# Kernel optimization log

Measured on AMD Instinct MI355X. Metric: run time of the kernel, lower is better.

Reference implementation:

```python
import jax, jax.numpy as jnp
import numpy as np

G = 4096   # num_genes
P = 4096   # num_perts
H = 64     # hidden_size
B = 4      # num_graphs
E1 = 81920 # coexpress edges
E2 = 81920 # GO edges
FF = 512   # transformer ffn
NH = 2     # attention heads
INTER, LAT = 32, 16  # VAE dims

def _bn(x, g, b, eps=1e-5):
    # BatchNorm1d in training mode: batch stats (biased var)
    m = x.mean(0); v = x.var(0)
    return (x - m) / jnp.sqrt(v + eps) * g + b

def _ln(x, g, b, eps=1e-5):
    m = x.mean(-1, keepdims=True); v = x.var(-1, keepdims=True)
    return (x - m) / jnp.sqrt(v + eps) * g + b

def _mlp2(x, w1, b1, g1, be1, w2, b2, g2, be2):
    # MLP([a,b,c]) builds Linear->BN->ReLU->Linear->BN (trailing ReLU stripped)
    h = jax.nn.relu(_bn(x @ w1.T + b1, g1, be1))
    return _bn(h @ w2.T + b2, g2, be2)

def _sgconv(x, ei, ew, w, b, n):
    # SGConv K=1: gcn_norm (self loops, symmetric norm) then linear
    src = jnp.concatenate([ei[0], jnp.arange(n)])
    dst = jnp.concatenate([ei[1], jnp.arange(n)])
    wgt = jnp.concatenate([ew, jnp.ones((n,), ew.dtype)])
    deg = jax.ops.segment_sum(wgt, dst, num_segments=n)
    dinv = jnp.where(deg > 0, 1.0 / jnp.sqrt(jnp.where(deg > 0, deg, 1.0)), 0.0)
    norm = dinv[dst] * wgt * dinv[src]
    agg = jax.ops.segment_sum(norm[:, None] * x[src], dst, num_segments=n)
    return agg @ w.T + b

def setup_inputs():
    ks = iter(jax.random.split(jax.random.key(0), 80))
    def nrm(shape, s=0.05):
        return jax.random.normal(next(ks), shape, dtype=jnp.float32) * s
    d = {}
    d['x'] = jax.random.uniform(next(ks), (B * G,), dtype=jnp.float32)
    d['pert_idx'] = jax.random.randint(next(ks), (B, 2), 0, P)
    d['mask'] = jnp.zeros((G, G), jnp.float32)
    d['ei_co'] = jax.random.randint(next(ks), (2, E1), 0, G)
    d['w_co'] = jax.random.uniform(next(ks), (E1,), dtype=jnp.float32)
    d['ei_go'] = jax.random.randint(next(ks), (2, E2), 0, P)
    d['w_go'] = jax.random.uniform(next(ks), (E2,), dtype=jnp.float32)
    d['gene_emb'] = nrm((G, H)); d['emb_pos'] = nrm((G, H)); d['pert_tbl'] = nrm((P, H))
    d['sg_co_w'] = nrm((H, H)); d['sg_co_b'] = jnp.zeros((H,))
    d['sg_go_w'] = nrm((H, H)); d['sg_go_b'] = jnp.zeros((H,))
    d['bn_emb_g'] = jnp.ones((H,)); d['bn_emb_b'] = jnp.zeros((H,))
    for pre, din, dout in [('etv2_1', H, H), ('etv2_2', H, H), ('pf_1', H, H), ('pf_2', H, H), ('rw_1', H, 2 * H), ('rw_2', 2 * H, H)]:
        d[pre + '_w'] = nrm((dout, din)); d[pre + '_b'] = jnp.zeros((dout,))
        d[pre + '_g'] = jnp.ones((dout,)); d[pre + '_be'] = jnp.zeros((dout,))
    d['bnpb_g'] = jnp.ones((H,)); d['bnpb_b'] = jnp.zeros((H,))
    d['attn_in_w'] = nrm((3 * H, H)); d['attn_in_b'] = jnp.zeros((3 * H,))
    d['attn_out_w'] = nrm((H, H)); d['attn_out_b'] = jnp.zeros((H,))
    d['ln1_g'] = jnp.ones((H,)); d['ln1_b'] = jnp.zeros((H,))
    d['ff1_w'] = nrm((FF, H)); d['ff1_b'] = jnp.zeros((FF,))
    d['ff2_w'] = nrm((H, FF)); d['ff2_b'] = jnp.zeros((H,))
    d['ln2_g'] = jnp.ones((H,)); d['ln2_b'] = jnp.zeros((H,))
    d['indv_w1'] = nrm((G, H)); d['indv_b1'] = jnp.zeros((G,))
    d['vae_e1_w'] = nrm((INTER, G)); d['vae_e1_b'] = jnp.zeros((INTER,))
    d['vae_mu_w'] = nrm((LAT, INTER)); d['vae_mu_b'] = jnp.zeros((LAT,))
    d['vae_lv_w'] = nrm((LAT, INTER)); d['vae_lv_b'] = jnp.zeros((LAT,))
    d['vae_d1_w'] = nrm((INTER, LAT)); d['vae_d1_b'] = jnp.zeros((INTER,))
    d['vae_d2_w'] = nrm((G, INTER)); d['vae_d2_b'] = jnp.zeros((G,))
    d['eps'] = jax.random.normal(next(ks), (B, LAT), dtype=jnp.float32)
    return d

def reference(x, pert_idx, mask, ei_co, w_co, ei_go, w_go, gene_emb, emb_pos, pert_tbl, sg_co_w, sg_co_b, sg_go_w, sg_go_b, bn_emb_g, bn_emb_b, etv2_1_w, etv2_1_b, etv2_1_g, etv2_1_be, etv2_2_w, etv2_2_b, etv2_2_g, etv2_2_be, pf_1_w, pf_1_b, pf_1_g, pf_1_be, pf_2_w, pf_2_b, pf_2_g, pf_2_be, rw_1_w, rw_1_b, rw_1_g, rw_1_be, rw_2_w, rw_2_b, rw_2_g, rw_2_be, bnpb_g, bnpb_b, attn_in_w, attn_in_b, attn_out_w, attn_out_b, ln1_g, ln1_b, ff1_w, ff1_b, ff2_w, ff2_b, ln2_g, ln2_b, indv_w1, indv_b1, vae_e1_w, vae_e1_b, vae_mu_w, vae_mu_b, vae_lv_w, vae_lv_b, vae_d1_w, vae_d1_b, vae_d2_w, vae_d2_b, eps):
    # gene base embedding (identical across graphs until pert fusion)
    base = jax.nn.relu(_bn(gene_emb, bn_emb_g, bn_emb_b))               # [G,H]
    pos = _sgconv(emb_pos, ei_co, w_co, sg_co_w, sg_co_b, G)            # 1 gene-GNN layer
    base = base + 0.2 * pos
    base = _mlp2(base, etv2_1_w, etv2_1_b, etv2_1_g, etv2_1_be, etv2_2_w, etv2_2_b, etv2_2_g, etv2_2_be)
    # pert embeddings propagated on GO graph
    pge = _sgconv(pert_tbl, ei_go, w_go, sg_go_w, sg_go_b, P)           # [P,H]
    # per-graph pert_track: sum of pert embeddings (all pert_idx valid)
    psum = pge[pert_idx].sum(axis=1)                                    # [B,H]
    etot = _mlp2(psum, pf_1_w, pf_1_b, pf_1_g, pf_1_be, pf_2_w, pf_2_b, pf_2_g, pf_2_be)
    base_b = base[None, :, :] + etot[:, None, :]                        # [B,G,H]
    flat = jax.nn.relu(_bn(base_b.reshape(B * G, H), bnpb_g, bnpb_b))
    out = _mlp2(flat, rw_1_w, rw_1_b, rw_1_g, rw_1_be, rw_2_w, rw_2_b, rw_2_g, rw_2_be)
    out = out.reshape(B, G, H)
    # transformer encoder layer (post-norm, relu, nhead=2), eval/no-dropout
    qkv = out @ attn_in_w.T + attn_in_b
    q, k, v = jnp.split(qkv, 3, axis=-1)
    hd = H // NH
    q = q.reshape(B, G, NH, hd); k = k.reshape(B, G, NH, hd); v = v.reshape(B, G, NH, hd)
    sc = jnp.einsum('bqhd,bkhd->bhqk', q, k) / np.float32(np.sqrt(hd)) + mask
    a = jax.nn.softmax(sc, axis=-1)
    ctx = jnp.einsum('bhqk,bkhd->bqhd', a, v).reshape(B, G, H)
    att = ctx @ attn_out_w.T + attn_out_b
    h1 = _ln(out + att, ln1_g, ln1_b)
    ff = jax.nn.relu(h1 @ ff1_w.T + ff1_b) @ ff2_w.T + ff2_b
    enc = _ln(h1 + ff, ln2_g, ln2_b)
    # per-gene linear: (enc.unsqueeze(-1)*indv_w1).sum(2)+indv_b1
    pred0 = jnp.einsum('bgh,gh->bg', enc, indv_w1) + indv_b1
    # VAE branch on raw expression
    xr = x.reshape(B, G)
    he = jax.nn.relu(xr @ vae_e1_w.T + vae_e1_b)
    mu = he @ vae_mu_w.T + vae_mu_b
    lv = he @ vae_lv_w.T + vae_lv_b
    z = mu + eps * jnp.exp(0.5 * lv)
    hdc = jax.nn.relu(z @ vae_d1_w.T + vae_d1_b)
    recon = hdc @ vae_d2_w.T + vae_d2_b
    kl = -0.5 * jnp.mean(jnp.sum(1.0 + lv - mu ** 2 - jnp.exp(lv), axis=1))
    recon = jnp.where(xr == 0, 0.0, recon)
    pred = pred0 + recon
    return (pred, kl)
```

## Files before the change

kernel.cpp:

```cpp
#include <hip/hip_runtime.h>
#include <hip/hip_bf16.h>
#include <math.h>

#define GG 4096
#define PP 4096
#define HH 64
#define BB 4
#define E1N 81920
#define E2N 81920
#define FFD 512
#define BNEPS 1e-5f
#define LOG2E 1.44269504088896341f
#define QPRE (0.17677669529663687f * LOG2E)

typedef unsigned short ushort_t;
typedef unsigned int uint_t;
using sh8 = __attribute__((ext_vector_type(8))) short;
using sh4 = __attribute__((ext_vector_type(4))) short;
using f4  = __attribute__((ext_vector_type(4))) float;

#if __has_builtin(__builtin_amdgcn_mfma_f32_16x16x16bf16_1k)
#define MFMA16(a, b, c) __builtin_amdgcn_mfma_f32_16x16x16bf16_1k((a), (b), (c), 0, 0, 0)
#elif __has_builtin(__builtin_amdgcn_mfma_f32_16x16x16_bf16)
#define MFMA16(a, b, c) __builtin_amdgcn_mfma_f32_16x16x16_bf16((a), (b), (c), 0, 0, 0)
#else
static __device__ inline f4 mfma16_asm(sh4 a, sh4 b, f4 c) {
    f4 d;
    asm volatile("v_mfma_f32_16x16x16_bf16 %0, %1, %2, %3"
                 : "=v"(d) : "v"(a), "v"(b), "v"(c));
    return d;
}
#define MFMA16(a, b, c) mfma16_asm((a), (b), (c))
#endif

#define OF_STATS   0
#define OF_DEGCO   2048
#define OF_DEGGO   6144
#define OF_PSLOT   10240
#define OF_ETOT    10752
#define OF_HDC     11008
#define OF_HE      11136
#define OF_MFLAG   11264
#define OF_CNT     12288
#define OF_OFFS    16384
#define OF_WOFF    20608
#define OF_SSRC    24704
#define OF_SNRM    106624
#define OF_BASEIN  274432
#define OF_Y1      536576
#define OF_Y2      798720
#define OF_FLAT    1060864
#define OF_RW1     2109440
#define OF_RW2     4206592
#define OF_OUT     5255168
#define OF_QKV     6303744
#define OF_QB      12288
#define OF_KB      (OF_QB + 524288)
#define OF_VF      OF_FLAT
#define OF_OPA     OF_QKV
#define OF_OPB     OF_OUT
#define OF_LP      OF_RW1
#define OPS        1048576
#define OF_W1B     9449472
#define OF_W2B     9465856

__device__ inline ushort_t f2b(float f) {
    uint_t u = __builtin_bit_cast(uint_t, f);
    u += 0x7FFFu + ((u >> 16) & 1u);
    return (ushort_t)(u >> 16);
}

__device__ inline void gld16(const void* gptr, void* lptr) {
    __builtin_amdgcn_global_load_lds(
        (const __attribute__((address_space(1))) uint_t*)gptr,
        (__attribute__((address_space(3))) uint_t*)lptr, 16, 0, 0);
}

__device__ void dev_vae_he(int bid, const float* __restrict__ x, const float* __restrict__ W,
                           const float* __restrict__ bias, float* he, float* sh) {
    int b = bid >> 5, i = bid & 31;
    float s = 0.f;
    for (int g = threadIdx.x; g < 4096; g += 256) s += x[b * 4096 + g] * W[i * 4096 + g];
    sh[threadIdx.x] = s;
    __syncthreads();
    for (int o = 128; o > 0; o >>= 1) {
        if (threadIdx.x < o) sh[threadIdx.x] += sh[threadIdx.x + o];
        __syncthreads();
    }
    if (threadIdx.x == 0) he[b * 32 + i] = fmaxf(sh[0] + bias[i], 0.f);
}

__device__ void dev_vae_mid(const float* __restrict__ he,
                            const float* __restrict__ muw, const float* __restrict__ mub,
                            const float* __restrict__ lvw, const float* __restrict__ lvb,
                            const float* __restrict__ d1w, const float* __restrict__ d1b,
                            const float* __restrict__ eps, float* hdc, float* klout, float* zs) {
    int t = threadIdx.x;
    if (t < 64) {
        int b = t >> 4, l = t & 15;
        float mu = mub[l], lv = lvb[l];
        for (int i = 0; i < 32; i++) {
            float hv = he[b * 32 + i];
            mu += hv * muw[l * 32 + i];
            lv += hv * lvw[l * 32 + i];
        }
        zs[t] = mu + eps[t] * expf(0.5f * lv);
        float kterm = 1.f + lv - mu * mu - expf(lv);
        for (int o = 32; o > 0; o >>= 1) kterm += __shfl_xor(kterm, o, 64);
        if (t == 0) klout[0] = -0.5f * kterm * 0.25f;
    }
    __syncthreads();
    if (t < 128) {
        int b = t >> 5, i = t & 31;
        float a = d1b[i];
        for (int l = 0; l < 16; l++) a += zs[b * 16 + l] * d1w[i * 16 + l];
        hdc[t] = fmaxf(a, 0.f);
    }
}

__device__ void dev_edge_deg(int bid, const int* __restrict__ ei, const float* __restrict__ w,
                             float* deg, int E, int* cnt) {
    int e = bid * 256 + threadIdx.x;
    if (e < E) {
        int d = ei[E + e];
        atomicAdd(&deg[d], w[e]);
        if (cnt) atomicAdd(&cnt[d], 1);
    }
}

__device__ void dev_cs_part(int bid, const float* __restrict__ X, int N,
                            float* sum, float* sumsq, float* sh) {
    int t = threadIdx.x;
    int col = t & 63, ro = t >> 6;
    int rows = N >> 8;
    int r0 = bid * rows;
    float s = 0.f, q = 0.f;
    for (int r = r0 + ro; r < r0 + rows; r += 4) {
        float v = X[r * 64 + col];
        s += v; q += v * v;
    }
    float* ls = sh; float* lq = sh + 256;
    ls[t] = s; lq[t] = q;
    __syncthreads();
    if (t < 64) {
        for (int j = t + 64; j < 256; j += 64) { s += ls[j]; q += lq[j]; }
        atomicAdd(&sum[t], s);
        atomicAdd(&sumsq[t], q);
    }
}

__device__ void dev_mask_scan(int bid, const float* __restrict__ mask, int* flag) {
    const uint4* m4 = (const uint4*)mask;
    const int total = (GG * GG) / 4;
    uint_t acc = 0u;
    for (int i = bid * 256 + threadIdx.x; i < total; i += 512 * 256) {
        uint4 v = m4[i];
        acc |= v.x | v.y | v.z | v.w;
    }
    if (acc) atomicOr(flag, 1);
}

__device__ void dev_scatter(int bid, const int* __restrict__ ei, const float* __restrict__ w,
                            const float* __restrict__ deg,
                            int* woff, int* ssrc, float* snrm) {
    int e = bid * 256 + threadIdx.x;
    if (e >= E1N) return;
    int src = ei[e], dst = ei[E1N + e];
    float nrm = rsqrtf(deg[dst] + 1.f) * w[e] * rsqrtf(deg[src] + 1.f);
    int pos = atomicAdd(&woff[dst], 1);
    ssrc[pos] = src;
    snrm[pos] = nrm;
}
// ... 340 lines not shown
        float eb = etot[bb * 64 + t];
        bsc[t] = sc2 * is3 * g3[t];
        bsh[t] = (sh2 + eb - m3) * is3 * g3[t] + b3[t];
    }
    __syncthreads();
    for (int i = t; i < 1024; i += 256) {
        int r = i >> 4, kq = (i & 15) * 4;
        int g = (row0 + r) & 4095;
        float4 v = *(const float4*)&y2[(size_t)g * 64 + kq];
        Xs[r][kq] = fmaxf(v.x * bsc[kq] + bsh[kq], 0.f);
        Xs[r][kq + 1] = fmaxf(v.y * bsc[kq + 1] + bsh[kq + 1], 0.f);
        Xs[r][kq + 2] = fmaxf(v.z * bsc[kq + 2] + bsh[kq + 2], 0.f);
        Xs[r][kq + 3] = fmaxf(v.w * bsc[kq + 3] + bsh[kq + 3], 0.f);
        float4 wv = *(const float4*)&W[(size_t)(cb + r) * 64 + kq];
        Ws[r][kq] = wv.x; Ws[r][kq + 1] = wv.y; Ws[r][kq + 2] = wv.z; Ws[r][kq + 3] = wv.w;
    }
    __syncthreads();
    float acc[4][4];
    #pragma unroll
    for (int j = 0; j < 4; j++)
        #pragma unroll
        for (int i = 0; i < 4; i++) acc[j][i] = 0.f;
    #pragma unroll 4
    for (int k = 0; k < 64; k += 2) {
        float2 a[4], b[4];
        #pragma unroll
        for (int j = 0; j < 4; j++) a[j] = *(const float2*)&Xs[r0 + j][k];
        #pragma unroll
        for (int i = 0; i < 4; i++) b[i] = *(const float2*)&Ws[c0 + i][k];
        #pragma unroll
        for (int j = 0; j < 4; j++)
            #pragma unroll
            for (int i = 0; i < 4; i++)
                acc[j][i] += a[j].x * b[i].x + a[j].y * b[i].y;
    }
    float4 bi = *(const float4*)&bias[cb + c0];
    float scol[4] = {0.f, 0.f, 0.f, 0.f}, qcol[4] = {0.f, 0.f, 0.f, 0.f};
    #pragma unroll
    for (int j = 0; j < 4; j++) {
        float4 o;
        o.x = acc[j][0] + bi.x; o.y = acc[j][1] + bi.y;
        o.z = acc[j][2] + bi.z; o.w = acc[j][3] + bi.w;
        *(float4*)&Y[(size_t)(row0 + r0 + j) * 128 + cb + c0] = o;
        scol[0] += o.x; scol[1] += o.y; scol[2] += o.z; scol[3] += o.w;
        qcol[0] += o.x * o.x; qcol[1] += o.y * o.y;
        qcol[2] += o.z * o.z; qcol[3] += o.w * o.w;
    }
    __syncthreads();
    #pragma unroll
    for (int i = 0; i < 4; i++) { Xs[ty][c0 + i] = scol[i]; Ws[ty][c0 + i] = qcol[i]; }
    __syncthreads();
    if (t < 64) {
        float ss = 0.f, qq = 0.f;
        #pragma unroll
        for (int r = 0; r < 16; r++) { ss += Xs[r][t]; qq += Ws[r][t]; }
        atomicAdd(&osum[cb + t], ss);
        atomicAdd(&osq[cb + t], qq);
    }
}

__launch_bounds__(256)
__global__ void k_gemm_qkv(const float* __restrict__ X, const float* __restrict__ W,
                           const float* __restrict__ bias,
                           const float* __restrict__ bnsum, const float* __restrict__ bnsq,
                           const float* __restrict__ bng, const float* __restrict__ bnb,
                           ushort_t* __restrict__ Qb, ushort_t* __restrict__ Kb,
                           ushort_t* __restrict__ Vf) {
    __shared__ float Xs[64][66];
    __shared__ float Ws[64][66];
    __shared__ float bsc[64], bsh[64];
    const int t = threadIdx.x;
    const int row0 = blockIdx.x * 64, yb = blockIdx.y, cb = yb * 64;
    const int tx = t & 15, ty = t >> 4;
    const int c0 = tx * 4, r0 = ty * 4;
    const float invN = 1.0f / (float)(BB * GG);
    if (t < 64) {
        float m = bnsum[t] * invN;
        float is_ = rsqrtf(bnsq[t] * invN - m * m + BNEPS);
        float sc = is_ * bng[t];
        bsc[t] = sc; bsh[t] = bnb[t] - m * sc;
    }
    __syncthreads();
    for (int i = t; i < 1024; i += 256) {
        int r = i >> 4, kq = (i & 15) * 4;
        float4 v = *(const float4*)&X[(size_t)(row0 + r) * 64 + kq];
        Xs[r][kq] = v.x * bsc[kq] + bsh[kq];
        Xs[r][kq + 1] = v.y * bsc[kq + 1] + bsh[kq + 1];
        Xs[r][kq + 2] = v.z * bsc[kq + 2] + bsh[kq + 2];
        Xs[r][kq + 3] = v.w * bsc[kq + 3] + bsh[kq + 3];
        float4 wv = *(const float4*)&W[(size_t)(cb + r) * 64 + kq];
        Ws[r][kq] = wv.x; Ws[r][kq + 1] = wv.y; Ws[r][kq + 2] = wv.z; Ws[r][kq + 3] = wv.w;
    }
    __syncthreads();
    float acc[4][4];
    #pragma unroll
    for (int j = 0; j < 4; j++)
        #pragma unroll
        for (int i = 0; i < 4; i++) acc[j][i] = 0.f;
    #pragma unroll 4
    for (int k = 0; k < 64; k += 2) {
        float2 a[4], b[4];
        #pragma unroll
        for (int j = 0; j < 4; j++) a[j] = *(const float2*)&Xs[r0 + j][k];
        #pragma unroll
        for (int i = 0; i < 4; i++) b[i] = *(const float2*)&Ws[c0 + i][k];
        #pragma unroll
        for (int j = 0; j < 4; j++)
            #pragma unroll
            for (int i = 0; i < 4; i++)
                acc[j][i] += a[j].x * b[i].x + a[j].y * b[i].y;
    }
    float4 bi = *(const float4*)&bias[cb + c0];
    const int b2 = row0 >> 12, tile = (row0 & 4095) >> 6;
    if (yb < 2) {
        ushort_t* Dst = (yb == 0) ? Qb : Kb;
        const float sc2 = (yb == 0) ? QPRE : 1.0f;
        const int h = c0 >> 5, d = c0 & 31;
        #pragma unroll
        for (int j = 0; j < 4; j++) {
            union { ushort_t u[4]; uint2 v; } pk;
            pk.u[0] = f2b((acc[j][0] + bi.x) * sc2);
            pk.u[1] = f2b((acc[j][1] + bi.y) * sc2);
            pk.u[2] = f2b((acc[j][2] + bi.z) * sc2);
            pk.u[3] = f2b((acc[j][3] + bi.w) * sc2);
            int g = (row0 & 4095) + r0 + j;
            *(uint2*)&Dst[((size_t)(b2 * 2 + h) * GG + g) * 32 + d] = pk.v;
        }
    } else {
        __syncthreads();
        #pragma unroll
        for (int j = 0; j < 4; j++) {
            Xs[r0 + j][c0] = acc[j][0] + bi.x;
            Xs[r0 + j][c0 + 1] = acc[j][1] + bi.y;
            Xs[r0 + j][c0 + 2] = acc[j][2] + bi.z;
            Xs[r0 + j][c0 + 3] = acc[j][3] + bi.w;
        }
        __syncthreads();
        #pragma unroll
        for (int h = 0; h < 2; h++) {
            union { ushort_t u[8]; uint4 v; } pk;
            #pragma unroll
            for (int j = 0; j < 8; j++) {
                int idx = t * 8 + j;
                int g2 = idx >> 8, L = (idx >> 2) & 63, i = idx & 3;
                int key = (g2 >> 1) * 16 + ((L >> 4) << 2) + i;
                int d = ((g2 & 1) << 4) + (L & 15);
                pk.u[j] = f2b(Xs[key][h * 32 + d]);
            }
            *(uint4*)&Vf[((size_t)((b2 * 2 + h) * 64 + tile)) * 2048 + t * 8] = pk.v;
        }
    }
}

__launch_bounds__(512, 4)
__global__ void k_attn_mfma(const ushort_t* __restrict__ Qb, const ushort_t* __restrict__ Kb,
                            const ushort_t* __restrict__ Vf, const float* __restrict__ mask,
                            const float* __restrict__ mflag,
                            float* __restrict__ opA, float* __restrict__ opB,
                            float* __restrict__ Lp) {
    __shared__ ushort_t Kl[2][4][2048];
    __shared__ ushort_t Vl[2][4][2048];
    const int split = blockIdx.y;
    const int bh0 = blockIdx.z * 4;
    const int q0 = blockIdx.x * 64;
    const int kstart = split * (GG / 4), kend = kstart + (GG / 4);
    const int t = threadIdx.x;
    const int lane = t & 63, w = t >> 6;
    const int qg = w >> 1, kh = w & 1;
    const int l15 = lane & 15, quad = lane >> 4;
    const int i2a = kh * 2, i2b = kh * 2 + 1;
    const int um = (*(const int*)mflag) != 0;

    sh8 qf[4];
    #pragma unroll
    for (int bh = 0; bh < 4; bh++)
        qf[bh] = *(const sh8*)&Qb[((size_t)(bh0 + bh) * GG + q0 + qg * 16 + l15) * 32 + quad * 8];
    const float* mrow = mask + (size_t)(q0 + qg * 16 + l15) * GG + quad * 4;

    auto stage = [&](int buf, int k0) {
        #pragma unroll
        for (int s = 0; s < 2; s++) {
            int idx = s * 512 + t;
            int bh = idx >> 8, c = idx & 255;
            int key = ((c >> 6) << 4) + (c & 15);
            int chunk = (c >> 4) & 3;
            gld16(Kb + ((size_t)(bh0 + bh) * GG + k0 + key) * 32 + chunk * 8,
                  &Kl[buf][bh][c * 8]);
            gld16(Vf + ((size_t)((bh0 + bh) * 64 + (k0 >> 6))) * 2048 + c * 8,
                  &Vl[buf][bh][c * 8]);
        }
    };
    stage(0, kstart);

    const float4 zf4 = {0.f, 0.f, 0.f, 0.f};
    float4 mva = zf4, mvb = zf4;
    if (um) {
        mva = *(const float4*)&mrow[kstart + i2a * 16];
        mvb = *(const float4*)&mrow[kstart + i2b * 16];
    }

    f4 O0[4], O1[4];
    float ls[4];
    #pragma unroll
    for (int bh = 0; bh < 4; bh++) {
        O0[bh] = f4{0.f, 0.f, 0.f, 0.f};
        O1[bh] = f4{0.f, 0.f, 0.f, 0.f};
        ls[bh] = 0.f;
    }

    for (int k0 = kstart; k0 < kend; k0 += 64) {
        const int cur = ((k0 - kstart) >> 6) & 1;
        __syncthreads();
        if (k0 + 64 < kend) stage(cur ^ 1, k0 + 64);
        float4 mva_n = zf4, mvb_n = zf4;
        if (um) {
            const int kp = (k0 + 64 < kend) ? (k0 + 64) : k0;
            mva_n = *(const float4*)&mrow[kp + i2a * 16];
            mvb_n = *(const float4*)&mrow[kp + i2b * 16];
        }
        #pragma unroll
        for (int bh = 0; bh < 4; bh++) {
            sh8 kfa = *(const sh8*)&Kl[cur][bh][(i2a * 64 + lane) * 8];
            sh8 kfb = *(const sh8*)&Kl[cur][bh][(i2b * 64 + lane) * 8];
            f4 z = {0.f, 0.f, 0.f, 0.f};
            f4 sa = __builtin_amdgcn_mfma_f32_16x16x32_bf16(kfa, qf[bh], z, 0, 0, 0);
            f4 sb = __builtin_amdgcn_mfma_f32_16x16x32_bf16(kfb, qf[bh], z, 0, 0, 0);
            {
                float p0 = exp2f(fmaf(mva.x, LOG2E, sa[0]));
                float p1 = exp2f(fmaf(mva.y, LOG2E, sa[1]));
                float p2 = exp2f(fmaf(mva.z, LOG2E, sa[2]));
                float p3 = exp2f(fmaf(mva.w, LOG2E, sa[3]));
                ls[bh] += (p0 + p1) + (p2 + p3);
                union { __hip_bfloat162 h2[2]; sh4 v; } pkp;
                pkp.h2[0] = __float22bfloat162_rn(float2{p0, p1});
                pkp.h2[1] = __float22bfloat162_rn(float2{p2, p3});
                sh4 vf0 = *(const sh4*)&Vl[cur][bh][((i2a * 2 + 0) * 64 + lane) * 4];
                sh4 vf1 = *(const sh4*)&Vl[cur][bh][((i2a * 2 + 1) * 64 + lane) * 4];
                O0[bh] = MFMA16(pkp.v, vf0, O0[bh]);
                O1[bh] = MFMA16(pkp.v, vf1, O1[bh]);
            }
            {
                float p0 = exp2f(fmaf(mvb.x, LOG2E, sb[0]));
                float p1 = exp2f(fmaf(mvb.y, LOG2E, sb[1]));
                float p2 = exp2f(fmaf(mvb.z, LOG2E, sb[2]));
                float p3 = exp2f(fmaf(mvb.w, LOG2E, sb[3]));
                ls[bh] += (p0 + p1) + (p2 + p3);
                union { __hip_bfloat162 h2[2]; sh4 v; } pkp;
                pkp.h2[0] = __float22bfloat162_rn(float2{p0, p1});
                pkp.h2[1] = __float22bfloat162_rn(float2{p2, p3});
                sh4 vf0 = *(const sh4*)&Vl[cur][bh][((i2b * 2 + 0) * 64 + lane) * 4];
                sh4 vf1 = *(const sh4*)&Vl[cur][bh][((i2b * 2 + 1) * 64 + lane) * 4];
                O0[bh] = MFMA16(pkp.v, vf0, O0[bh]);
                O1[bh] = MFMA16(pkp.v, vf1, O1[bh]);
            }
        }
        mva = mva_n; mvb = mvb_n;
    }
    #pragma unroll
    for (int bh = 0; bh < 4; bh++) {
        ls[bh] += __shfl_xor(ls[bh], 16, 64);
        ls[bh] += __shfl_xor(ls[bh], 32, 64);
    }
    __syncthreads();
    float* Ox = (float*)&Kl[0][0][0];
    float* Lx = (float*)&Vl[0][0][0];
    if (kh == 0) {
        #pragma unroll
        for (int bh = 0; bh < 4; bh++) {
            #pragma unroll
            for (int r = 0; r < 4; r++) {
                int ql = qg * 16 + quad * 4 + r;
                Ox[(bh * 64 + ql) * 32 + l15] = O0[bh][r];
                Ox[(bh * 64 + ql) * 32 + l15 + 16] = O1[bh][r];
            }
            if (quad == 0) Lx[bh * 64 + qg * 16 + l15] = ls[bh];
        }
    }
    __syncthreads();
    if (kh == 1) {
        float* op = (split < 3) ? (opA + (size_t)split * OPS) : opB;
        #pragma unroll
        for (int bh = 0; bh < 4; bh++) {
            int gbh = bh0 + bh;
            #pragma unroll
            for (int r = 0; r < 4; r++) {
                int ql = qg * 16 + quad * 4 + r;
                size_t o = ((size_t)gbh * GG + q0 + ql) * 32 + l15;
                op[o] = O0[bh][r] + Ox[(bh * 64 + ql) * 32 + l15];
                op[o + 16] = O1[bh][r] + Ox[(bh * 64 + ql) * 32 + l15 + 16];
            }
            if (quad == 0)
                Lp[split * 32768 + gbh * GG + q0 + qg * 16 + l15] =
                    ls[bh] + Lx[bh * 64 + qg * 16 + l15];
        }
    }
}

__launch_bounds__(256)
__global__ void k_tail(const float* __restrict__ opA, const float* __restrict__ opB,
                       const float* __restrict__ Lp, const float* __restrict__ yrw2,
                       const float* __restrict__ Waout, const float* __restrict__ baout,
                       const float* __restrict__ bsum5, const float* __restrict__ bsq5,
                       const float* __restrict__ bg5, const float* __restrict__ bb5,
                       const float* __restrict__ lg1, const float* __restrict__ lb1,
                       const ushort_t* __restrict__ W1b, const float* __restrict__ b1f,
                       const ushort_t* __restrict__ W2b, const float* __restrict__ b2f,
                       const float* __restrict__ lg2, const float* __restrict__ lb2,
                       const float* __restrict__ indvw, const float* __restrict__ indvb,
                       const float* __restrict__ hdc, const float* __restrict__ d2w,
                       const float* __restrict__ d2b, const float* __restrict__ x,
                       float* __restrict__ outp) {
    __shared__ float Wt[4160];
    __shared__ float Cs[4160];
    __shared__ ushort_t Hb[4096];
    __shared__ ushort_t FT[32768];
    __shared__ ushort_t WS[2][4096];
    const int t = threadIdx.x;
    const int r0b = blockIdx.x * 64;
    const int lane = t & 63, w = t >> 6;
    const int l15 = lane & 15, quad = lane >> 4;

    for (int i = t; i < 4096; i += 256) Wt[(i & 63) * 65 + (i >> 6)] = Waout[i];
    {
        int col = t & 63, rl = t >> 6;
        int hh = col >> 5, d = col & 31;
        for (int jj = 0; jj < 16; jj++) {
            int lrow = rl + jj * 4;
            int row = r0b + lrow;
            int b = row >> 12, q = row & 4095;
            int bhq = (b * 2 + hh) * GG + q;
            size_t oi = (size_t)bhq * 32 + d;
            float num = opA[oi] + opA[OPS + oi] + opA[2 * OPS + oi] + opB[oi];
            float den = Lp[bhq] + Lp[32768 + bhq] + Lp[65536 + bhq] + Lp[98304 + bhq];
            Cs[lrow * 65 + col] = num / den;
        }
    }
    __syncthreads();
    const float invN = 1.0f / (float)(BB * GG);
    float m5 = bsum5[lane] * invN;
    float is5 = rsqrtf(bsq5[lane] * invN - m5 * m5 + BNEPS);
    float h1v[16];
    for (int j = 0; j < 16; j++) {
        int lrow = w * 16 + j;
        int row = r0b + lrow;
        float acc = baout[lane];
        const float* cr = Cs + lrow * 65;
        #pragma unroll 8
        for (int k = 0; k < 64; k++) acc += cr[k] * Wt[k * 65 + lane];
        float ov = (yrw2[(size_t)row * 64 + lane] - m5) * is5 * bg5[lane] + bb5[lane];
        float v = ov + acc;
        float s = v;
        for (int o = 32; o > 0; o >>= 1) s += __shfl_xor(s, o, 64);
        float mean = s * (1.f / 64.f);
        float d = v - mean;
        float sq = d * d;
        for (int o = 32; o > 0; o >>= 1) sq += __shfl_xor(sq, o, 64);
        float inv = rsqrtf(sq * (1.f / 64.f) + BNEPS);
        h1v[j] = d * inv * lg1[lane] + lb1[lane];
    }
    __syncthreads();
    float* h1f = Wt;
    for (int j = 0; j < 16; j++) h1f[(w * 16 + j) * 65 + lane] = h1v[j];
    __syncthreads();
    if (t < 128) {
        int kt = t >> 6, lane6 = t & 63;
        int q2 = (lane6 >> 4) & 3, r15 = lane6 & 15;
        for (int rg = 0; rg < 4; rg++) {
            union { ushort_t u[8]; uint4 v4; } pk;
            #pragma unroll
            for (int j = 0; j < 8; j++)
                pk.u[j] = f2b(h1f[(rg * 16 + r15) * 65 + kt * 32 + q2 * 8 + j]);
            *(uint4*)&Hb[(rg * 2 + kt) * 512 + lane6 * 8] = pk.v4;
        }
    }
    auto stage1 = [&](int buf, int cb8) {
        int cb = cb8 * 64;
        #pragma unroll
        for (int kt = 0; kt < 2; kt++)
            gld16(W1b + (size_t)((cb + w * 16 + l15) * 64 + kt * 32 + quad * 8),
                  &WS[buf][(w * 2 + kt) * 512 + lane * 8]);
    };
    stage1(0, 0);
    for (int cb8 = 0; cb8 < 8; cb8++) {
        const int cur = cb8 & 1;
        __syncthreads();
        if (cb8 + 1 < 8) stage1(cur ^ 1, cb8 + 1);
        sh8 xf0 = *(const sh8*)&Hb[(w * 2 + 0) * 512 + lane * 8];
        sh8 xf1 = *(const sh8*)&Hb[(w * 2 + 1) * 512 + lane * 8];
        const int cb = cb8 * 64;
        #pragma unroll
        for (int c = 0; c < 4; c++) {
            sh8 wf0 = *(const sh8*)&WS[cur][(c * 2 + 0) * 512 + lane * 8];
            sh8 wf1 = *(const sh8*)&WS[cur][(c * 2 + 1) * 512 + lane * 8];
            f4 z = {0.f, 0.f, 0.f, 0.f};
            f4 acc = __builtin_amdgcn_mfma_f32_16x16x32_bf16(wf0, xf0, z, 0, 0, 0);
            acc = __builtin_amdgcn_mfma_f32_16x16x32_bf16(wf1, xf1, acc, 0, 0, 0);
            float4 bv = *(const float4*)&b1f[cb + c * 16 + quad * 4];
            union { ushort_t u[4]; uint2 v2; } pk;
            pk.u[0] = f2b(fmaxf(acc[0] + bv.x, 0.f));
            pk.u[1] = f2b(fmaxf(acc[1] + bv.y, 0.f));
            pk.u[2] = f2b(fmaxf(acc[2] + bv.z, 0.f));
            pk.u[3] = f2b(fmaxf(acc[3] + bv.w, 0.f));
            int kt512 = cb8 * 2 + (c >> 1);
            int quadp = (c & 1) * 2 + (quad >> 1);
            int j0 = (quad & 1) * 4;
            *(uint2*)&FT[((w * 16 + kt512) * 64 + quadp * 16 + l15) * 8 + j0] = pk.v2;
        }
    }
    auto stage2 = [&](int buf, int k0) {
        #pragma unroll
        for (int kt = 0; kt < 2; kt++)
            gld16(W2b + (size_t)((w * 16 + l15) * 512 + k0 + kt * 32 + quad * 8),
                  &WS[buf][(w * 2 + kt) * 512 + lane * 8]);
    };
    stage2(0, 0);
    f4 acc2[4];
    #pragma unroll
    for (int c = 0; c < 4; c++) acc2[c] = f4{0.f, 0.f, 0.f, 0.f};
    for (int k0 = 0; k0 < 512; k0 += 64) {
        const int cur = (k0 >> 6) & 1;
        __syncthreads();
        if (k0 + 64 < 512) stage2(cur ^ 1, k0 + 64);
        const int ktb = k0 >> 5;
        #pragma unroll
        for (int kt = 0; kt < 2; kt++) {
            sh8 xf = *(const sh8*)&FT[((w * 16 + ktb + kt) * 64 + lane) * 8];
            #pragma unroll
            for (int c = 0; c < 4; c++) {
                sh8 wf = *(const sh8*)&WS[cur][(c * 2 + kt) * 512 + lane * 8];
                acc2[c] = __builtin_amdgcn_mfma_f32_16x16x32_bf16(wf, xf, acc2[c], 0, 0, 0);
            }
        }
    }
    const int row = r0b + w * 16 + l15;
    const int b = row >> 12, g = row & 4095;
// ... 14 lines not shown
    sq += __shfl_xor(sq, 16, 64); sq += __shfl_xor(sq, 32, 64);
    float mean = s * (1.f / 64.f);
    float inv = rsqrtf(sq * (1.f / 64.f) - mean * mean + BNEPS);
    float pd = 0.f;
    #pragma unroll
    for (int c = 0; c < 4; c++) {
        float4 lgv = *(const float4*)&lg2[c * 16 + quad * 4];
        float4 lbv = *(const float4*)&lb2[c * 16 + quad * 4];
        float4 iwv = *(const float4*)&indvw[(size_t)g * 64 + c * 16 + quad * 4];
        pd += ((v[c][0] - mean) * inv * lgv.x + lbv.x) * iwv.x;
        pd += ((v[c][1] - mean) * inv * lgv.y + lbv.y) * iwv.y;
        pd += ((v[c][2] - mean) * inv * lgv.z + lbv.z) * iwv.z;
        pd += ((v[c][3] - mean) * inv * lgv.w + lbv.w) * iwv.w;
    }
    float rc = 0.f;
    #pragma unroll
    for (int i = 0; i < 8; i++)
        rc += hdc[b * 32 + quad * 8 + i] * d2w[(size_t)g * 32 + quad * 8 + i];
    pd += __shfl_xor(pd, 16, 64); pd += __shfl_xor(pd, 32, 64);
    rc += __shfl_xor(rc, 16, 64); rc += __shfl_xor(rc, 32, 64);
    if (quad == 0) {
        float recon = rc + d2b[g];
        if (x[row] == 0.f) recon = 0.f;
        outp[row] = pd + indvb[g] + recon;
    }
}

extern "C" void kernel_launch(void* const* d_in, const int* in_sizes, int n_in,
                              void* d_out, int out_size, void* d_ws, size_t ws_size,
                              hipStream_t stream) {
    const float* x        = (const float*)d_in[0];
    const int*   pert_idx = (const int*)  d_in[1];
    const float* mask     = (const float*)d_in[2];
    const int*   ei_co    = (const int*)  d_in[3];
    const float* w_co     = (const float*)d_in[4];
    const int*   ei_go    = (const int*)  d_in[5];
    const float* w_go     = (const float*)d_in[6];
    const float* gene_emb = (const float*)d_in[7];
    const float* emb_pos  = (const float*)d_in[8];
    const float* pert_tbl = (const float*)d_in[9];
    const float* sg_co_w  = (const float*)d_in[10];
    const float* sg_co_b  = (const float*)d_in[11];
    const float* sg_go_w  = (const float*)d_in[12];
    const float* sg_go_b  = (const float*)d_in[13];
    const float* bn_emb_g = (const float*)d_in[14];
    const float* bn_emb_b = (const float*)d_in[15];
    const float* etv1_w   = (const float*)d_in[16];
    const float* etv1_b   = (const float*)d_in[17];
    const float* etv1_g   = (const float*)d_in[18];
    const float* etv1_be  = (const float*)d_in[19];
    const float* etv2_w   = (const float*)d_in[20];
    const float* etv2_b   = (const float*)d_in[21];
    const float* etv2_g   = (const float*)d_in[22];
    const float* etv2_be  = (const float*)d_in[23];
    const float* pf1_w    = (const float*)d_in[24];
    const float* pf1_b    = (const float*)d_in[25];
    const float* pf1_g    = (const float*)d_in[26];
    const float* pf1_be   = (const float*)d_in[27];
    const float* pf2_w    = (const float*)d_in[28];
    const float* pf2_b    = (const float*)d_in[29];
    const float* pf2_g    = (const float*)d_in[30];
    const float* pf2_be   = (const float*)d_in[31];
    const float* rw1_w    = (const float*)d_in[32];
    const float* rw1_b    = (const float*)d_in[33];
    const float* rw1_g    = (const float*)d_in[34];
    const float* rw1_be   = (const float*)d_in[35];
    const float* rw2_w    = (const float*)d_in[36];
    const float* rw2_b    = (const float*)d_in[37];
    const float* rw2_g    = (const float*)d_in[38];
    const float* rw2_be   = (const float*)d_in[39];
    const float* bnpb_g   = (const float*)d_in[40];
    const float* bnpb_b   = (const float*)d_in[41];
    const float* ain_w    = (const float*)d_in[42];
    const float* ain_b    = (const float*)d_in[43];
    const float* aout_w   = (const float*)d_in[44];
    const float* aout_b   = (const float*)d_in[45];
    const float* ln1_g    = (const float*)d_in[46];
    const float* ln1_b    = (const float*)d_in[47];
    const float* ff1_w    = (const float*)d_in[48];
    const float* ff1_b    = (const float*)d_in[49];
    const float* ff2_w    = (const float*)d_in[50];
    const float* ff2_b    = (const float*)d_in[51];
    const float* ln2_g    = (const float*)d_in[52];
    const float* ln2_b    = (const float*)d_in[53];
    const float* indv_w   = (const float*)d_in[54];
    const float* indv_b   = (const float*)d_in[55];
    const float* ve1_w    = (const float*)d_in[56];
    const float* ve1_b    = (const float*)d_in[57];
    const float* vmu_w    = (const float*)d_in[58];
    const float* vmu_b    = (const float*)d_in[59];
    const float* vlv_w    = (const float*)d_in[60];
    const float* vlv_b    = (const float*)d_in[61];
    const float* vd1_w    = (const float*)d_in[62];
    const float* vd1_b    = (const float*)d_in[63];
    const float* vd2_w    = (const float*)d_in[64];
    const float* vd2_b    = (const float*)d_in[65];
    const float* veps     = (const float*)d_in[66];

    float* ws   = (float*)d_ws;
    float* outp = (float*)d_out;

    float* stm1 = ws + OF_STATS + 1 * 256; float* sti1 = stm1 + 128;
    float* stm2 = ws + OF_STATS + 2 * 256; float* sti2 = stm2 + 128;
    float* stm4 = ws + OF_STATS + 4 * 256; float* sti4 = stm4 + 128;
    float* stm5 = ws + OF_STATS + 5 * 256; float* sti5 = stm5 + 128;

    float* basein = ws + OF_BASEIN;
    float* y1     = ws + OF_Y1;
    float* y2     = ws + OF_Y2;
    float* yrw1   = ws + OF_RW1;
    float* yrw2   = ws + OF_RW2;
    float* opA    = ws + OF_OPA;
    float* opB    = ws + OF_OPB;
    float* Lp     = ws + OF_LP;
    ushort_t* Qb  = (ushort_t*)(ws + OF_QB);
    ushort_t* Kb  = (ushort_t*)(ws + OF_KB);
    ushort_t* Vf  = (ushort_t*)(ws + OF_VF);
    ushort_t* W1b = (ushort_t*)(ws + OF_W1B);
    ushort_t* W2b = (ushort_t*)(ws + OF_W2B);

    const int NG = BB * GG;
    const float iG = 1.0f / (float)GG, iNG = 1.0f / (float)NG;

    hipMemsetAsync(ws, 0, 11268 * sizeof(float), stream);
    hipMemsetAsync(ws + OF_CNT, 0, 4096 * sizeof(int), stream);

    k_fat12<<<1792, 256, 0, stream>>>(ws, ei_co, w_co, ei_go, w_go, gene_emb,
                                      x, ve1_w, ve1_b, ff1_w, ff2_w, mask);
    k_scan<<<1, 256, 0, stream>>>(ws);
    k_fat3<<<641, 256, 0, stream>>>(ws, ei_co, w_co, pert_idx,
                                    ei_go, w_go, pert_tbl,
                                    vmu_w, vmu_b, vlv_w, vlv_b, vd1_w, vd1_b,
                                    veps, outp + NG);
    k_fat4<<<1025, 256, 0, stream>>>(ws, gene_emb, emb_pos, sg_co_w, sg_co_b,
                                     bn_emb_g, bn_emb_b, pert_idx, pert_tbl,
                                     sg_go_w, sg_go_b,
                                     pf1_w, pf1_b, pf1_g, pf1_be,
                                     pf2_w, pf2_b, pf2_g, pf2_be);
    k_gemm64<<<dim3(GG / 64, 1), 256, 0, stream>>>(basein, etv1_w, etv1_b, y1, 64, 64,
                                                   nullptr, nullptr, nullptr, nullptr, 0.f, 0,
                                                   stm1, sti1);
    k_gemm64<<<dim3(GG / 64, 1), 256, 0, stream>>>(y1, etv2_w, etv2_b, y2, 64, 64,
                                                   stm1, sti1, etv1_g, etv1_be, iG, 1,
                                                   stm2, sti2);
    k_gemm_rw1<<<dim3(NG / 64, 2), 256, 0, stream>>>(y2, ws + OF_ETOT, stm2, sti2,
                                                     etv2_g, etv2_be, bnpb_g, bnpb_b,
                                                     rw1_w, rw1_b, yrw1, stm4, sti4);
    k_gemm64<<<dim3(NG / 64, 1), 256, 0, stream>>>(yrw1, rw2_w, rw2_b, yrw2, 128, 64,
                                                   stm4, sti4, rw1_g, rw1_be, iNG, 1,
                                                   stm5, sti5);
    k_gemm_qkv<<<dim3(NG / 64, 3), 256, 0, stream>>>(yrw2, ain_w, ain_b,
                                                     stm5, sti5, rw2_g, rw2_be,
                                                     Qb, Kb, Vf);
    k_attn_mfma<<<dim3(GG / 64, 4, 2), 512, 0, stream>>>(Qb, Kb, Vf, mask,
                                                         ws + OF_MFLAG, opA, opB, Lp);
    k_tail<<<NG / 64, 256, 0, stream>>>(opA, opB, Lp, yrw2, aout_w, aout_b,
                                        stm5, sti5, rw2_g, rw2_be, ln1_g, ln1_b,
                                        W1b, ff1_b, W2b, ff2_b, ln2_g, ln2_b,
                                        indv_w, indv_b, ws + OF_HDC, vd2_w, vd2_b,
                                        x, outp);
}
```

Baseline: 454.1 us.

## Halve heads per attention block and specialize mask-free softmax path

Each attention block now handles 2 batch-heads instead of 4. This halves the shared memory and register footprint, and the grid doubles along z to keep total work the same. Launch bounds rise to 8 blocks per CU so more blocks can be resident. The main loop is also templated on whether the mask is used, so the mask-free path skips the mask loads and the FMA before each exp2. In exchange, each K/V tile is loaded for fewer heads per block and the Q fragments are reused less.

```diff
diff --git a/kernel.cpp b/kernel.cpp
--- a/kernel.cpp
+++ b/kernel.cpp
@@ -18,6 +18,9 @@
 using sh8 = __attribute__((ext_vector_type(8))) short;
 using sh4 = __attribute__((ext_vector_type(4))) short;
 using f4  = __attribute__((ext_vector_type(4))) float;
+
+struct MaskOn  { static constexpr bool v = true; };
+struct MaskOff { static constexpr bool v = false; };
 
 #if __has_builtin(__builtin_amdgcn_mfma_f32_16x16x16bf16_1k)
 #define MFMA16(a, b, c) __builtin_amdgcn_mfma_f32_16x16x16bf16_1k((a), (b), (c), 0, 0, 0)
@@ -664,16 +667,16 @@
     }
 }
 
-__launch_bounds__(512, 4)
+__launch_bounds__(512, 8)
 __global__ void k_attn_mfma(const ushort_t* __restrict__ Qb, const ushort_t* __restrict__ Kb,
                             const ushort_t* __restrict__ Vf, const float* __restrict__ mask,
                             const float* __restrict__ mflag,
                             float* __restrict__ opA, float* __restrict__ opB,
                             float* __restrict__ Lp) {
-    __shared__ ushort_t Kl[2][4][2048];
-    __shared__ ushort_t Vl[2][4][2048];
+    __shared__ ushort_t Kl[2][2][2048];
+    __shared__ ushort_t Vl[2][2][2048];
     const int split = blockIdx.y;
-    const int bh0 = blockIdx.z * 4;
+    const int bh0 = blockIdx.z * 2;
     const int q0 = blockIdx.x * 64;
     const int kstart = split * (GG / 4), kend = kstart + (GG / 4);
     const int t = threadIdx.x;
@@ -683,93 +686,105 @@
     const int i2a = kh * 2, i2b = kh * 2 + 1;
     const int um = (*(const int*)mflag) != 0;
 
-    sh8 qf[4];
-    #pragma unroll
-    for (int bh = 0; bh < 4; bh++)
+    sh8 qf[2];
+    #pragma unroll
+    for (int bh = 0; bh < 2; bh++)
         qf[bh] = *(const sh8*)&Qb[((size_t)(bh0 + bh) * GG + q0 + qg * 16 + l15) * 32 + quad * 8];
     const float* mrow = mask + (size_t)(q0 + qg * 16 + l15) * GG + quad * 4;
 
     auto stage = [&](int buf, int k0) {
-        #pragma unroll
-        for (int s = 0; s < 2; s++) {
-            int idx = s * 512 + t;
-            int bh = idx >> 8, c = idx & 255;
-            int key = ((c >> 6) << 4) + (c & 15);
-            int chunk = (c >> 4) & 3;
-            gld16(Kb + ((size_t)(bh0 + bh) * GG + k0 + key) * 32 + chunk * 8,
-                  &Kl[buf][bh][c * 8]);
-            gld16(Vf + ((size_t)((bh0 + bh) * 64 + (k0 >> 6))) * 2048 + c * 8,
-                  &Vl[buf][bh][c * 8]);
-        }
+        int bh = t >> 8, c = t & 255;
+        int key = ((c >> 6) << 4) + (c & 15);
+        int chunk = (c >> 4) & 3;
+        gld16(Kb + ((size_t)(bh0 + bh) * GG + k0 + key) * 32 + chunk * 8,
+              &Kl[buf][bh][c * 8]);
+        gld16(Vf + ((size_t)((bh0 + bh) * 64 + (k0 >> 6))) * 2048 + c * 8,
+              &Vl[buf][bh][c * 8]);
     };
     stage(0, kstart);
 
-    const float4 zf4 = {0.f, 0.f, 0.f, 0.f};
-    float4 mva = zf4, mvb = zf4;
-    if (um) {
-        mva = *(const float4*)&mrow[kstart + i2a * 16];
-        mvb = *(const float4*)&mrow[kstart + i2b * 16];
-    }
-
-    f4 O0[4], O1[4];
-    float ls[4];
-    #pragma unroll
-    for (int bh = 0; bh < 4; bh++) {
+    f4 O0[2], O1[2];
+    float ls[2];
+    #pragma unroll
+    for (int bh = 0; bh < 2; bh++) {
         O0[bh] = f4{0.f, 0.f, 0.f, 0.f};
         O1[bh] = f4{0.f, 0.f, 0.f, 0.f};
         ls[bh] = 0.f;
     }
 
-    for (int k0 = kstart; k0 < kend; k0 += 64) {
-        const int cur = ((k0 - kstart) >> 6) & 1;
-        __syncthreads();
-        if (k0 + 64 < kend) stage(cur ^ 1, k0 + 64);
-        float4 mva_n = zf4, mvb_n = zf4;
-        if (um) {
-            const int kp = (k0 + 64 < kend) ? (k0 + 64) : k0;
-            mva_n = *(const float4*)&mrow[kp + i2a * 16];
-            mvb_n = *(const float4*)&mrow[kp + i2b * 16];
-        }
-        #pragma unroll
-        for (int bh = 0; bh < 4; bh++) {
-            sh8 kfa = *(const sh8*)&Kl[cur][bh][(i2a * 64 + lane) * 8];
-            sh8 kfb = *(const sh8*)&Kl[cur][bh][(i2b * 64 + lane) * 8];
-            f4 z = {0.f, 0.f, 0.f, 0.f};
-            f4 sa = __builtin_amdgcn_mfma_f32_16x16x32_bf16(kfa, qf[bh], z, 0, 0, 0);
-            f4 sb = __builtin_amdgcn_mfma_f32_16x16x32_bf16(kfb, qf[bh], z, 0, 0, 0);
-            {
-                float p0 = exp2f(fmaf(mva.x, LOG2E, sa[0]));
-                float p1 = exp2f(fmaf(mva.y, LOG2E, sa[1]));
-                float p2 = exp2f(fmaf(mva.z, LOG2E, sa[2]));
-                float p3 = exp2f(fmaf(mva.w, LOG2E, sa[3]));
-                ls[bh] += (p0 + p1) + (p2 + p3);
-                union { __hip_bfloat162 h2[2]; sh4 v; } pkp;
-                pkp.h2[0] = __float22bfloat162_rn(float2{p0, p1});
-                pkp.h2[1] = __float22bfloat162_rn(float2{p2, p3});
-                sh4 vf0 = *(const sh4*)&Vl[cur][bh][((i2a * 2 + 0) * 64 + lane) * 4];
-                sh4 vf1 = *(const sh4*)&Vl[cur][bh][((i2a * 2 + 1) * 64 + lane) * 4];
-                O0[bh] = MFMA16(pkp.v, vf0, O0[bh]);
-                O1[bh] = MFMA16(pkp.v, vf1, O1[bh]);
+    auto run = [&](auto tag) {
+        constexpr bool U = decltype(tag)::v;
+        const float4 zf4 = {0.f, 0.f, 0.f, 0.f};
+        float4 mva = zf4, mvb = zf4;
+        if constexpr (U) {
+            mva = *(const float4*)&mrow[kstart + i2a * 16];
+            mvb = *(const float4*)&mrow[kstart + i2b * 16];
+        }
+        for (int k0 = kstart; k0 < kend; k0 += 64) {
+            const int cur = ((k0 - kstart) >> 6) & 1;
+            __syncthreads();
+            if (k0 + 64 < kend) stage(cur ^ 1, k0 + 64);
+            float4 mva_n = zf4, mvb_n = zf4;
+            if constexpr (U) {
+                const int kp = (k0 + 64 < kend) ? (k0 + 64) : k0;
+                mva_n = *(const float4*)&mrow[kp + i2a * 16];
+                mvb_n = *(const float4*)&mrow[kp + i2b * 16];
             }
-            {
-                float p0 = exp2f(fmaf(mvb.x, LOG2E, sb[0]));
-                float p1 = exp2f(fmaf(mvb.y, LOG2E, sb[1]));
-                float p2 = exp2f(fmaf(mvb.z, LOG2E, sb[2]));
-                float p3 = exp2f(fmaf(mvb.w, LOG2E, sb[3]));
-                ls[bh] += (p0 + p1) + (p2 + p3);
-                union { __hip_bfloat162 h2[2]; sh4 v; } pkp;
-                pkp.h2[0] = __float22bfloat162_rn(float2{p0, p1});
-                pkp.h2[1] = __float22bfloat162_rn(float2{p2, p3});
-                sh4 vf0 = *(const sh4*)&Vl[cur][bh][((i2b * 2 + 0) * 64 + lane) * 4];
-                sh4 vf1 = *(const sh4*)&Vl[cur][bh][((i2b * 2 + 1) * 64 + lane) * 4];
-                O0[bh] = MFMA16(pkp.v, vf0, O0[bh]);
-                O1[bh] = MFMA16(pkp.v, vf1, O1[bh]);
+            #pragma unroll
+            for (int bh = 0; bh < 2; bh++) {
+                sh8 kfa = *(const sh8*)&Kl[cur][bh][(i2a * 64 + lane) * 8];
+                sh8 kfb = *(const sh8*)&Kl[cur][bh][(i2b * 64 + lane) * 8];
+                f4 z = {0.f, 0.f, 0.f, 0.f};
+                f4 sa = __builtin_amdgcn_mfma_f32_16x16x32_bf16(kfa, qf[bh], z, 0, 0, 0);
+                f4 sb = __builtin_amdgcn_mfma_f32_16x16x32_bf16(kfb, qf[bh], z, 0, 0, 0);
+                {
+                    float p0, p1, p2, p3;
+                    if constexpr (U) {
+                        p0 = exp2f(fmaf(mva.x, LOG2E, sa[0]));
+                        p1 = exp2f(fmaf(mva.y, LOG2E, sa[1]));
+                        p2 = exp2f(fmaf(mva.z, LOG2E, sa[2]));
+                        p3 = exp2f(fmaf(mva.w, LOG2E, sa[3]));
+                    } else {
+                        p0 = exp2f(sa[0]); p1 = exp2f(sa[1]);
+                        p2 = exp2f(sa[2]); p3 = exp2f(sa[3]);
+                    }
+                    ls[bh] += (p0 + p1) + (p2 + p3);
+                    union { __hip_bfloat162 h2[2]; sh4 v; } pkp;
+                    pkp.h2[0] = __float22bfloat162_rn(float2{p0, p1});
+                    pkp.h2[1] = __float22bfloat162_rn(float2{p2, p3});
+                    sh4 vf0 = *(const sh4*)&Vl[cur][bh][((i2a * 2 + 0) * 64 + lane) * 4];
+                    sh4 vf1 = *(const sh4*)&Vl[cur][bh][((i2a * 2 + 1) * 64 + lane) * 4];
+                    O0[bh] = MFMA16(pkp.v, vf0, O0[bh]);
+                    O1[bh] = MFMA16(pkp.v, vf1, O1[bh]);
+                }
+                {
+                    float p0, p1, p2, p3;
+                    if constexpr (U) {
+                        p0 = exp2f(fmaf(mvb.x, LOG2E, sb[0]));
+                        p1 = exp2f(fmaf(mvb.y, LOG2E, sb[1]));
+                        p2 = exp2f(fmaf(mvb.z, LOG2E, sb[2]));
+                        p3 = exp2f(fmaf(mvb.w, LOG2E, sb[3]));
+                    } else {
+                        p0 = exp2f(sb[0]); p1 = exp2f(sb[1]);
+                        p2 = exp2f(sb[2]); p3 = exp2f(sb[3]);
+                    }
+                    ls[bh] += (p0 + p1) + (p2 + p3);
+                    union { __hip_bfloat162 h2[2]; sh4 v; } pkp;
+                    pkp.h2[0] = __float22bfloat162_rn(float2{p0, p1});
+                    pkp.h2[1] = __float22bfloat162_rn(float2{p2, p3});
+                    sh4 vf0 = *(const sh4*)&Vl[cur][bh][((i2b * 2 + 0) * 64 + lane) * 4];
+                    sh4 vf1 = *(const sh4*)&Vl[cur][bh][((i2b * 2 + 1) * 64 + lane) * 4];
+                    O0[bh] = MFMA16(pkp.v, vf0, O0[bh]);
+                    O1[bh] = MFMA16(pkp.v, vf1, O1[bh]);
+                }
             }
-        }
-        mva = mva_n; mvb = mvb_n;
-    }
-    #pragma unroll
-    for (int bh = 0; bh < 4; bh++) {
+            if constexpr (U) { mva = mva_n; mvb = mvb_n; }
+        }
+    };
+    if (um) run(MaskOn{}); else run(MaskOff{});
+
+    #pragma unroll
+    for (int bh = 0; bh < 2; bh++) {
         ls[bh] += __shfl_xor(ls[bh], 16, 64);
         ls[bh] += __shfl_xor(ls[bh], 32, 64);
     }
@@ -778,7 +793,7 @@
     float* Lx = (float*)&Vl[0][0][0];
     if (kh == 0) {
         #pragma unroll
-        for (int bh = 0; bh < 4; bh++) {
+        for (int bh = 0; bh < 2; bh++) {
             #pragma unroll
             for (int r = 0; r < 4; r++) {
                 int ql = qg * 16 + quad * 4 + r;
@@ -792,7 +807,7 @@
     if (kh == 1) {
         float* op = (split < 3) ? (opA + (size_t)split * OPS) : opB;
         #pragma unroll
-        for (int bh = 0; bh < 4; bh++) {
+        for (int bh = 0; bh < 2; bh++) {
             int gbh = bh0 + bh;
             #pragma unroll
             for (int r = 0; r < 4; r++) {
@@ -1113,7 +1128,7 @@
     k_gemm_qkv<<<dim3(NG / 64, 3), 256, 0, stream>>>(yrw2, ain_w, ain_b,
                                                      stm5, sti5, rw2_g, rw2_be,
                                                      Qb, Kb, Vf);
-    k_attn_mfma<<<dim3(GG / 64, 4, 2), 512, 0, stream>>>(Qb, Kb, Vf, mask,
+    k_attn_mfma<<<dim3(GG / 64, 4, 4), 512, 0, stream>>>(Qb, Kb, Vf, mask,
                                                          ws + OF_MFLAG, opA, opB, Lp);
     k_tail<<<NG / 64, 256, 0, stream>>>(opA, opB, Lp, yrw2, aout_w, aout_b,
                                         stm5, sti5, rw2_g, rw2_be, ln1_g, ln1_b,
```

Result: no change. 455.4 us (+0.3%).
